# Optimization experiments

Hardware: AMD Instinct MI355X
Metric: run time of the kernel (lower is better)

The kernel has to match this reference:

```python
import jax, jax.numpy as jnp
import numpy as np

IN_DIM, R = 80, 5
MEL = IN_DIM * R          # 400
H = 256                   # hidden size used everywhere
PRE2 = 128                # prenet second layer
B, T_ENC, T_DEC = 16, 384, 200


def _gru(x, h, wih, whh, bih, bhh):
    """torch.nn.GRUCell math."""
    gi = x @ wih.T + bih
    gh = h @ whh.T + bhh
    ir, iz, inn = jnp.split(gi, 3, axis=-1)
    hr, hz, hn = jnp.split(gh, 3, axis=-1)
    r = jax.nn.sigmoid(ir + hr)
    z = jax.nn.sigmoid(iz + hz)
    n = jnp.tanh(inn + r * hn)
    return (1.0 - z) * n + z * h


def setup_inputs() -> dict:
    key = jax.random.key(0)
    ks = jax.random.split(key, 32)
    p = lambda k, shape: jax.random.normal(k, shape, dtype=jnp.float32) * 0.05
    inp = {
        "encoder_outputs": jax.random.normal(ks[0], (B, T_ENC, H), dtype=jnp.float32),
        "inputs": jax.random.normal(ks[1], (B, T_DEC, MEL), dtype=jnp.float32),
        "memory_lengths": jax.random.randint(ks[2], (B,), T_ENC // 2, T_ENC + 1, dtype=jnp.int32),
        # prenet: Linear(400,256) -> relu -> Linear(256,128) -> relu (dropout omitted = eval mode)
        "prenet_w1": p(ks[3], (H, MEL)), "prenet_b1": p(ks[4], (H,)),
        "prenet_w2": p(ks[5], (PRE2, H)), "prenet_b2": p(ks[6], (PRE2,)),
        # memory_layer: Linear(256,256,bias=False)
        "mem_w": p(ks[7], (H, H)),
        # attention GRUCell(256+128 -> 256)
        "attn_gru_wih": p(ks[8], (3 * H, H + PRE2)), "attn_gru_whh": p(ks[9], (3 * H, H)),
        "attn_gru_bih": p(ks[10], (3 * H,)), "attn_gru_bhh": p(ks[11], (3 * H,)),
        # BahdanauAttention: query_layer Linear(256,256,bias=False), v Linear(256,1,bias=False)
        "attn_q_w": p(ks[12], (H, H)), "attn_v": p(ks[13], (H,)),
        # project_to_decoder_in: Linear(512,256)
        "proj_in_w": p(ks[14], (H, 2 * H)), "proj_in_b": p(ks[15], (H,)),
        # two decoder GRUCells(256,256), stacked on leading axis
        "dec_wih": p(ks[16], (2, 3 * H, H)), "dec_whh": p(ks[17], (2, 3 * H, H)),
        "dec_bih": p(ks[18], (2, 3 * H)), "dec_bhh": p(ks[19], (2, 3 * H)),
        # proj_to_mel: Linear(256,400)
        "mel_w": p(ks[20], (MEL, H)), "mel_b": p(ks[21], (MEL,)),
    }
    return inp


def reference(encoder_outputs, inputs, memory_lengths,
              prenet_w1, prenet_b1, prenet_w2, prenet_b2, mem_w,
              attn_gru_wih, attn_gru_whh, attn_gru_bih, attn_gru_bhh,
              attn_q_w, attn_v, proj_in_w, proj_in_b,
              dec_wih, dec_whh, dec_bih, dec_bhh, mel_w, mel_b):
    b, t_enc, d = encoder_outputs.shape
    processed_memory = encoder_outputs @ mem_w.T                # (B,T_enc,256)
    pad_mask = jnp.arange(t_enc)[None, :] >= memory_lengths[:, None]  # True = padded

    # teacher forcing: step t consumes inputs[t-1], step 0 consumes zeros
    shifted = jnp.concatenate([jnp.zeros_like(inputs[:, :1]), inputs[:, :-1]], axis=1)
    xs = jnp.swapaxes(shifted, 0, 1)                            # (T_dec,B,400)

    def step(carry, x):
        attn_h, attention, d1, d2 = carry
        # prenet (eval mode: dropout disabled)
        pn = jax.nn.relu(x @ prenet_w1.T + prenet_b1)
        pn = jax.nn.relu(pn @ prenet_w2.T + prenet_b2)           # (B,128)
        # attention GRU cell on [prenet_out, prev_attention]
        cell_in = jnp.concatenate([pn, attention], axis=-1)      # (B,384)
        attn_h = _gru(cell_in, attn_h, attn_gru_wih, attn_gru_whh,
                      attn_gru_bih, attn_gru_bhh)                # (B,256)
        # Bahdanau additive attention
        pq = attn_h @ attn_q_w.T                                 # (B,256)
        e = jnp.tanh(pq[:, None, :] + processed_memory) @ attn_v  # (B,T_enc)
        e = jnp.where(pad_mask, -jnp.inf, e)
        align = jax.nn.softmax(e, axis=-1)
        attention = jnp.einsum('bt,btd->bd', align, encoder_outputs)  # (B,256)
        # decoder input projection + 2 residual GRU cells
        dec_in = jnp.concatenate([attn_h, attention], axis=-1) @ proj_in_w.T + proj_in_b
        hs = [d1, d2]
        for i in range(2):
            hs[i] = _gru(dec_in, hs[i], dec_wih[i], dec_whh[i], dec_bih[i], dec_bhh[i])
            dec_in = hs[i] + dec_in
        out = dec_in @ mel_w.T + mel_b                           # (B,400)
        return (attn_h, attention, hs[0], hs[1]), (out, align)

    z = jnp.zeros((b, d), dtype=encoder_outputs.dtype)
    init = (z, z, z, z)
    _, (outs, aligns) = jax.lax.scan(step, init, xs)
    outputs = jnp.swapaxes(outs, 0, 1)                           # (B,T_dec,400)
    alignments = jnp.swapaxes(aligns, 0, 1)                      # (B,T_dec,T_enc)
    return outputs, alignments
```

## Files before the change

kernel.cpp:

```cpp
#include <hip/hip_runtime.h>
#include <math.h>

#define TID ((int)threadIdx.x)
#define BID ((int)blockIdx.x)

typedef float4 f4;

constexpr int NB   = 16;
constexpr int TENC = 384;
constexpr int TDEC = 200;
constexpr int HD   = 256;
constexpr int MELD = 400;
constexpr int P2   = 128;
constexpr int G3   = 768;

constexpr int OFF_PM     = 0;
constexpr int OFF_GIPN   = OFF_PM     + NB*TENC*HD;
constexpr int OFF_PN1    = OFF_GIPN   + TDEC*G3*NB;
constexpr int OFF_PN2    = OFF_PN1    + TDEC*HD*NB;
constexpr int OFF_D2O    = OFF_PN2    + TDEC*P2*NB;
constexpr int OFF_ATTNH  = OFF_D2O    + TDEC*HD*NB;
constexpr int OFF_CTX    = OFF_ATTNH  + 2*4096;
constexpr int OFF_D1     = OFF_CTX    + 3*4096;
constexpr int OFF_D2     = OFF_D1     + 2*4096;
constexpr int OFF_DECIN  = OFF_D2     + 4096;
constexpr int OFF_DECIN1 = OFF_DECIN  + 4096;
constexpr int OFF_GI     = OFF_DECIN1 + 4096;
constexpr int OFF_GH     = OFF_GI     + 12288;
constexpr int OFF_GI1    = OFF_GH     + 12288;
constexpr int OFF_GH1    = OFF_GI1    + 12288;
constexpr int OFF_GI2    = OFF_GH1    + 12288;
constexpr int OFF_GH2    = OFF_GI2    + 12288;
constexpr int OFF_PQ     = OFF_GH2    + 12288;
constexpr int OFF_E      = OFF_PQ     + 4096;
constexpr int OFF_W1T    = OFF_E      + 6144;
constexpr int OFF_W2T    = OFF_W1T    + 102400;
constexpr int OFF_WMEMT  = OFF_W2T    + 32768;
constexpr int OFF_WPNT   = OFF_WMEMT  + 65536;
constexpr int OFF_WATTT  = OFF_WPNT   + 98304;
constexpr int OFF_WHHT   = OFF_WATTT  + 196608;
constexpr int OFF_WQT    = OFF_WHHT   + 196608;
constexpr int OFF_WPROJT = OFF_WQT    + 65536;
constexpr int OFF_WIH1T  = OFF_WPROJT + 131072;
constexpr int OFF_WHH1T  = OFF_WIH1T  + 196608;
constexpr int OFF_WIH2T  = OFF_WHH1T  + 196608;
constexpr int OFF_WHH2T  = OFF_WIH2T  + 196608;
constexpr int OFF_WMELT  = OFF_WHH2T  + 196608;

__device__ __forceinline__ float sigf(float x){ return 1.f/(1.f+__expf(-x)); }
__device__ __forceinline__ float tanhf_(float x){
  x = fminf(15.f, fmaxf(-15.f, x));
  float e = __expf(2.f*x);
  return (e-1.f)/(e+1.f);
}

__global__ void k_init(float* ws){
  int g = BID*256 + TID;
  for (int idx = g; idx < 32768; idx += 32*256) ws[OFF_ATTNH + idx] = 0.f;
}

__global__ void k_tr(const float* pw1, const float* pw2, const float* wmem,
                     const float* gwih, const float* gwhh, const float* qw,
                     const float* pjw, const float* dwih, const float* dwhh,
                     const float* mw, float* ws){
  int g = BID*256 + TID;
  if (g < 102400){ int j=g%256,k=g/256; ws[OFF_W1T+g]=pw1[j*400+k]; return;} g-=102400;
  if (g < 32768){ int j=g%128,k=g/128; ws[OFF_W2T+g]=pw2[j*256+k]; return;} g-=32768;
  if (g < 65536){ int j=g%256,k=g/256; ws[OFF_WMEMT+g]=wmem[j*256+k]; return;} g-=65536;
  if (g < 98304){ int j=g%768,k=g/768; ws[OFF_WPNT+g]=gwih[j*384+k]; return;} g-=98304;
  if (g < 196608){ int j=g%768,k=g/768; ws[OFF_WATTT+g]=gwih[j*384+128+k]; return;} g-=196608;
  if (g < 196608){ int j=g%768,k=g/768; ws[OFF_WHHT+g]=gwhh[j*256+k]; return;} g-=196608;
  if (g < 65536){ int j=g%256,k=g/256; ws[OFF_WQT+g]=qw[j*256+k]; return;} g-=65536;
  if (g < 131072){ int j=g%256,k=g/256; ws[OFF_WPROJT+g]=pjw[j*512+k]; return;} g-=131072;
  if (g < 196608){ int j=g%768,k=g/768; ws[OFF_WIH1T+g]=dwih[j*256+k]; return;} g-=196608;
  if (g < 196608){ int j=g%768,k=g/768; ws[OFF_WHH1T+g]=dwhh[j*256+k]; return;} g-=196608;
  if (g < 196608){ int j=g%768,k=g/768; ws[OFF_WIH2T+g]=dwih[196608+j*256+k]; return;} g-=196608;
  if (g < 196608){ int j=g%768,k=g/768; ws[OFF_WHH2T+g]=dwhh[196608+j*256+k]; return;} g-=196608;
  if (g < 102400){ int j=g%400,k=g/400; ws[OFF_WMELT+g]=mw[j*256+k]; return;}
}

__global__ void k_pm(const float* __restrict__ enc, float* __restrict__ ws){
  int b = BID / 24, t0 = (BID % 24) * 16;
  int d = TID;
  const float* W = ws + OFF_WMEMT + d;
  const float* A = enc + (size_t)(b*TENC + t0)*HD;
  float acc[16];
  #pragma unroll
  for (int tt=0; tt<16; ++tt) acc[tt]=0.f;
  for (int k=0; k<HD; k+=4){
    float w0=W[(k+0)*256], w1=W[(k+1)*256], w2=W[(k+2)*256], w3=W[(k+3)*256];
    #pragma unroll
    for (int tt=0; tt<16; ++tt){
      f4 a = *(const f4*)(A + tt*HD + k);
      acc[tt] += w0*a.x + w1*a.y + w2*a.z + w3*a.w;
    }
  }
  float* P = ws + OFF_PM + (size_t)(b*TENC + t0)*HD + d;
  #pragma unroll
  for (int tt=0; tt<16; ++tt) P[tt*HD] = acc[tt];
}

__global__ void k_pre1(const float* __restrict__ inp, const float* __restrict__ pb1, float* __restrict__ ws){
  int t = BID >> 2;
  int j = ((BID & 3) * 64) + (TID & 63);
  int bq = TID >> 6;
  float b = pb1[j];
  float a0=b,a1=b,a2=b,a3=b;
  if (t > 0){
    const float* W = ws + OFF_W1T + j;
    const float* x0 = inp + (size_t)((bq*4+0)*TDEC + (t-1))*MELD;
    const float* x1 = inp + (size_t)((bq*4+1)*TDEC + (t-1))*MELD;
    const float* x2 = inp + (size_t)((bq*4+2)*TDEC + (t-1))*MELD;
    const float* x3 = inp + (size_t)((bq*4+3)*TDEC + (t-1))*MELD;
    for (int k=0;k<MELD;k+=4){
      float w0=W[(k+0)*256],w1=W[(k+1)*256],w2=W[(k+2)*256],w3=W[(k+3)*256];
      f4 v0=*(const f4*)(x0+k), v1=*(const f4*)(x1+k), v2=*(const f4*)(x2+k), v3=*(const f4*)(x3+k);
      a0 += w0*v0.x+w1*v0.y+w2*v0.z+w3*v0.w;
      a1 += w0*v1.x+w1*v1.y+w2*v1.z+w3*v1.w;
      a2 += w0*v2.x+w1*v2.y+w2*v2.z+w3*v2.w;
      a3 += w0*v3.x+w1*v3.y+w2*v3.z+w3*v3.w;
    }
  }
  f4 r; r.x=fmaxf(a0,0.f); r.y=fmaxf(a1,0.f); r.z=fmaxf(a2,0.f); r.w=fmaxf(a3,0.f);
  *(f4*)(ws + OFF_PN1 + (size_t)(t*HD + j)*NB + bq*4) = r;
}

__global__ void k_pre2(const float* __restrict__ pb2, float* __restrict__ ws){
  int t = BID >> 1;
  int j = ((BID & 1) * 64) + (TID & 63);
  int bq = TID >> 6;
  float b = pb2[j];
  f4 acc = {b,b,b,b};
  const float* W = ws + OFF_W2T + j;
  const float* A = ws + OFF_PN1 + (size_t)t*HD*NB + bq*4;
  #pragma unroll 4
  for (int k=0;k<HD;++k){
    float w = W[k*P2];
    f4 a = *(const f4*)(A + k*NB);
    acc.x += w*a.x; acc.y += w*a.y; acc.z += w*a.z; acc.w += w*a.w;
  }
  f4 r; r.x=fmaxf(acc.x,0.f); r.y=fmaxf(acc.y,0.f); r.z=fmaxf(acc.z,0.f); r.w=fmaxf(acc.w,0.f);
  *(f4*)(ws + OFF_PN2 + (size_t)(t*P2 + j)*NB + bq*4) = r;
}

__global__ void k_gipn(const float* __restrict__ gbih, float* __restrict__ ws){
  int t = BID / 12;
  int j = (BID % 12)*64 + (TID & 63);
  int bq = TID >> 6;
  float b = gbih[j];
  f4 acc = {b,b,b,b};
  const float* W = ws + OFF_WPNT + j;
  const float* A = ws + OFF_PN2 + (size_t)t*P2*NB + bq*4;
  #pragma unroll 4
  for (int k=0;k<P2;++k){
    float w = W[k*G3];
    f4 a = *(const f4*)(A + k*NB);
    acc.x += w*a.x; acc.y += w*a.y; acc.z += w*a.z; acc.w += w*a.w;
  }
  *(f4*)(ws + OFF_GIPN + (size_t)(t*G3 + j)*NB + bq*4) = acc;
}

__global__ void k1(float* __restrict__ ws, const float* __restrict__ gbhh,
                   const float* __restrict__ pjb, const float* __restrict__ dbhh, int i){
  __shared__ float as[4096];
  int lane = TID & 63, bq = TID >> 6;
  if (BID < 12){
    if (i >= TDEC) return;
    const float* cp = ws + OFF_CTX;
    #pragma unroll
    for (int e=0;e<16;++e){ int id = TID + e*256; as[id] = cp[id] + cp[id+4096] + cp[id+8192]; }
    __syncthreads();
    int j = BID*64 + lane;
    f4 acc = *(const f4*)(ws + OFF_GIPN + ((size_t)i*G3 + j)*NB + bq*4);
    const float* W = ws + OFF_WATTT + j;
    #pragma unroll 4
    for (int k=0;k<HD;++k){
      float w = W[k*G3];
      f4 a = *(const f4*)&as[k*NB + bq*4];
      acc.x += w*a.x; acc.y += w*a.y; acc.z += w*a.z; acc.w += w*a.w;
    }
    *(f4*)(ws + OFF_GI + j*NB + bq*4) = acc;
  } else if (BID < 24){
    if (i >= TDEC) return;
    int j = (BID-12)*64 + lane;
    float bb = gbhh[j];
    f4 acc = {bb,bb,bb,bb};
    const float* W = ws + OFF_WHHT + j;
    const float* A = ws + OFF_ATTNH + ((i+1)&1)*4096 + bq*4;
    #pragma unroll 4
    for (int k=0;k<HD;++k){
      float w = W[k*G3];
      f4 a = *(const f4*)(A + k*NB);
      acc.x += w*a.x; acc.y += w*a.y; acc.z += w*a.z; acc.w += w*a.w;
    }
    *(f4*)(ws + OFF_GH + j*NB + bq*4) = acc;
  } else if (BID < 28){
    if (i == 0) return;
    const float* cp = ws + OFF_CTX;
    #pragma unroll
    for (int e=0;e<16;++e){ int id = TID + e*256; as[id] = cp[id] + cp[id+4096] + cp[id+8192]; }
    __syncthreads();
    int row = (BID-24)*64 + lane;
    float bb = pjb[row];
    f4 acc = {bb,bb,bb,bb};
    const float* W = ws + OFF_WPROJT + row;
    const float* Ah = ws + OFF_ATTNH + ((i+1)&1)*4096 + bq*4;
    #pragma unroll 4
    for (int k=0;k<HD;++k){
      float w = W[k*HD];
      f4 a = *(const f4*)(Ah + k*NB);
      acc.x += w*a.x; acc.y += w*a.y; acc.z += w*a.z; acc.w += w*a.w;
    }
    #pragma unroll 4
    for (int k=0;k<HD;++k){
      float w = W[(k+HD)*HD];
      f4 a = *(const f4*)&as[k*NB + bq*4];
      acc.x += w*a.x; acc.y += w*a.y; acc.z += w*a.z; acc.w += w*a.w;
    }
    *(f4*)(ws + OFF_DECIN + row*NB + bq*4) = acc;
  } else if (BID < 40){
    if (i == 0) return;
    int j = (BID-28)*64 + lane;
    float bb = dbhh[G3 + j];
    f4 acc = {bb,bb,bb,bb};
    const float* W = ws + OFF_WHH2T + j;
    const float* A = ws + OFF_D2 + bq*4;
    #pragma unroll 4
    for (int k=0;k<HD;++k){
      float w = W[k*G3];
      f4 a = *(const f4*)(A + k*NB);
      acc.x += w*a.x; acc.y += w*a.y; acc.z += w*a.z; acc.w += w*a.w;
    }
    *(f4*)(ws + OFF_GH2 + j*NB + bq*4) = acc;
  }
}

__global__ void k2(float* __restrict__ ws, const float* __restrict__ dbih, int i){
  __shared__ float attns[4096];
  int lane = TID & 63, bq = TID >> 6;
  if (BID < 4){
    if (i >= TDEC) return;
    const float* gi = ws + OFF_GI; const float* gh = ws + OFF_GH;
    const float* hp = ws + OFF_ATTNH + ((i+1)&1)*4096;
    float* hn = ws + OFF_ATTNH + (i&1)*4096;
    #pragma unroll
    for (int e=0;e<16;++e){
      int id = TID + e*256;
      float ir=gi[id], iz=gi[id+4096], in_=gi[id+8192];
      float hr=gh[id], hz=gh[id+4096], hnn=gh[id+8192];
      float h = hp[id];
      float rr = sigf(ir+hr), zz = sigf(iz+hz);
      float nn = tanhf_(in_ + rr*hnn);
      float v = (1.f-zz)*nn + zz*h;
      attns[id] = v;
      if (BID==0) hn[id] = v;
    }
    __syncthreads();
    int row = BID*64 + lane;
    const float* W = ws + OFF_WQT + row;
    float a0=0.f,a1=0.f,a2=0.f,a3=0.f;
    #pragma unroll 4
    for (int k=0;k<HD;++k){
      float w = W[k*HD];
      f4 a = *(const f4*)&attns[k*NB + bq*4];
      a0 += w*a.x; a1 += w*a.y; a2 += w*a.z; a3 += w*a.w;
    }
    float* pq = ws + OFF_PQ;
    pq[(bq*4+0)*HD+row]=a0; pq[(bq*4+1)*HD+row]=a1;
    pq[(bq*4+2)*HD+row]=a2; pq[(bq*4+3)*HD+row]=a3;
  } else {
    if (i == 0) return;
    int j = (BID-4)*64 + lane;
    float bb = dbih[j];
    f4 acc = {bb,bb,bb,bb};
    const float* W = ws + OFF_WIH1T + j;
    const float* A = ws + OFF_DECIN + bq*4;
    #pragma unroll 4
    for (int k=0;k<HD;++k){
      float w = W[k*G3];
      f4 a = *(const f4*)(A + k*NB);
      acc.x += w*a.x; acc.y += w*a.y; acc.z += w*a.z; acc.w += w*a.w;
    }
    *(f4*)(ws + OFF_GI1 + j*NB + bq*4) = acc;
  }
}

__global__ void k4(float* __restrict__ ws, const float* __restrict__ av,
                   const int* __restrict__ mlen, const float* __restrict__ dbih, int i){
  __shared__ float sh[4096];
  if (BID < 48){
    if (i >= TDEC) return;
    int b = BID/3, ts = BID%3;
    int ks = TID >> 7, tt = TID & 127;
    int t = ts*128 + tt;
    const float* pmr = ws + OFF_PM + (size_t)(b*TENC + t)*HD + ks*128;
    const float* pqb = ws + OFF_PQ + b*HD + ks*128;
    const float* vv = av + ks*128;
    float s = 0.f;
    #pragma unroll 4
    for (int d=0; d<128; d+=4){
      f4 p = *(const f4*)(pmr+d);
      f4 q = *(const f4*)(pqb+d);
      f4 w = *(const f4*)(vv+d);
      s += w.x*tanhf_(p.x+q.x) + w.y*tanhf_(p.y+q.y)
         + w.z*tanhf_(p.z+q.z) + w.w*tanhf_(p.w+q.w);
    }
    sh[TID] = s; __syncthreads();
    if (TID < 128){
      float e = sh[TID] + sh[TID+128];
      int len = mlen[b];
      int tw = ts*128 + TID;
      ws[OFF_E + b*TENC + tw] = (tw < len) ? e : -1e30f;
    }
  } else {
    if (i == 0) return;
    int lane = TID & 63, bq = TID >> 6;
    const float* gi1 = ws + OFF_GI1; const float* gh1 = ws + OFF_GH1;
    const float* d1p = ws + OFF_D1 + (i&1)*4096;
    float* d1n = ws + OFF_D1 + ((i+1)&1)*4096;
    const float* din = ws + OFF_DECIN;
    float* din1 = ws + OFF_DECIN1;
    #pragma unroll
    for (int e=0;e<16;++e){
      int id = TID + e*256;
      float ir=gi1[id], iz=gi1[id+4096], in_=gi1[id+8192];
      float hr=gh1[id], hz=gh1[id+4096], hnn=gh1[id+8192];
      float h = d1p[id];
      float rr=sigf(ir+hr), zz=sigf(iz+hz);
      float nn=tanhf_(in_+rr*hnn);
      float dn = (1.f-zz)*nn + zz*h;
      float v = dn + din[id];
      sh[id] = v;
      if (BID==48){ d1n[id]=dn; din1[id]=v; }
    }
    __syncthreads();
    int j = (BID-48)*64 + lane;
    float bb = dbih[G3 + j];
    f4 acc = {bb,bb,bb,bb};
    const float* W = ws + OFF_WIH2T + j;
    #pragma unroll 4
    for (int k=0;k<HD;++k){
      float w = W[k*G3];
      f4 a = *(const f4*)&sh[k*NB + bq*4];
      acc.x += w*a.x; acc.y += w*a.y; acc.z += w*a.z; acc.w += w*a.w;
    }
    *(f4*)(ws + OFF_GI2 + j*NB + bq*4) = acc;
  }
}

__global__ void k5(float* __restrict__ ws, const float* __restrict__ enc,
                   const float* __restrict__ dbhh, float* __restrict__ out, int i){
  __shared__ float red[256];
  __shared__ float ps[128];
  if (BID < 48){
    if (i >= TDEC) return;
    int b = BID/3, ts = BID%3;
    const float* eb = ws + OFF_E + b*TENC;
    float m = -1e30f;
    for (int idx=TID; idx<TENC; idx+=256) m = fmaxf(m, eb[idx]);
    red[TID]=m; __syncthreads();
    for (int s=128; s>0; s>>=1){ if (TID<s) red[TID]=fmaxf(red[TID],red[TID+s]); __syncthreads(); }
    float M = red[0]; __syncthreads();
    float sl = 0.f;
    for (int idx=TID; idx<TENC; idx+=256) sl += __expf(eb[idx]-M);
    red[TID]=sl; __syncthreads();
    for (int s=128; s>0; s>>=1){ if (TID<s) red[TID]+=red[TID+s]; __syncthreads(); }
    float inv = 1.f/red[0];
    __syncthreads();
    if (TID < 128){
      int t = ts*128 + TID;
      float p = __expf(eb[t]-M)*inv;
      ps[TID] = p;
      out[1280000 + (size_t)(b*TDEC + i)*TENC + t] = p;
    }
    __syncthreads();
    const float* encb = enc + (size_t)(b*TENC + ts*128)*HD + TID;
    float ctx = 0.f;
    #pragma unroll 8
    for (int tt=0;tt<128;++tt) ctx += ps[tt]*encb[(size_t)tt*HD];
    ws[OFF_CTX + ts*4096 + TID*NB + b] = ctx;
  } else if (BID < 52){
    if (i == 0) return;
    const float* gi2 = ws+OFF_GI2; const float* gh2 = ws+OFF_GH2;
    float* d2 = ws+OFF_D2; const float* din1 = ws+OFF_DECIN1;
    float* d2o = ws + OFF_D2O + (size_t)(i-1)*4096;
    #pragma unroll
    for (int e=0;e<4;++e){
      int id = (BID-48)*1024 + e*256 + TID;
      float ir=gi2[id], iz=gi2[id+4096], in_=gi2[id+8192];
      float hr=gh2[id], hz=gh2[id+4096], hnn=gh2[id+8192];
      float h = d2[id];
      float rr=sigf(ir+hr), zz=sigf(iz+hz);
      float nn=tanhf_(in_+rr*hnn);
      float dn=(1.f-zz)*nn+zz*h;
      d2[id]=dn;
      d2o[id]=dn+din1[id];
    }
  } else {
    if (i >= TDEC) return;
    int lane=TID&63, bq=TID>>6;
    int j = (BID-52)*64 + lane;
    float bb = dbhh[j];
    f4 acc = {bb,bb,bb,bb};
    const float* W = ws+OFF_WHH1T+j;
    const float* A = ws+OFF_D1+((i+1)&1)*4096+bq*4;
    #pragma unroll 4
    for (int k=0;k<HD;++k){
      float w = W[k*G3];
      f4 a = *(const f4*)(A + k*NB);
      acc.x += w*a.x; acc.y += w*a.y; acc.z += w*a.z; acc.w += w*a.w;
    }
    *(f4*)(ws + OFF_GH1 + j*NB + bq*4) = acc;
  }
}

__global__ void k_mel(const float* __restrict__ ws, const float* __restrict__ mb, float* __restrict__ out){
  int t = BID/7, rb = (BID%7)*64;
  int j = rb + (TID&63), bq = TID>>6;
  if (j >= MELD) return;
  float bb = mb[j];
  f4 acc = {bb,bb,bb,bb};
  const float* W = ws + OFF_WMELT + j;
  const float* A = ws + OFF_D2O + (size_t)t*4096 + bq*4;
  #pragma unroll 4
  for (int k=0;k<HD;++k){
    float w = W[k*MELD];
    f4 a = *(const f4*)(A + k*NB);
    acc.x += w*a.x; acc.y += w*a.y; acc.z += w*a.z; acc.w += w*a.w;
  }
  out[(size_t)(bq*4+0)*80000 + t*MELD + j] = acc.x;
  out[(size_t)(bq*4+1)*80000 + t*MELD + j] = acc.y;
  out[(size_t)(bq*4+2)*80000 + t*MELD + j] = acc.z;
  out[(size_t)(bq*4+3)*80000 + t*MELD + j] = acc.w;
}

extern "C" void kernel_launch(void* const* d_in, const int* in_sizes, int n_in,
                              void* d_out, int out_size, void* d_ws, size_t ws_size,
                              hipStream_t stream) {
  const float* enc  = (const float*)d_in[0];
  const float* inp  = (const float*)d_in[1];
  const int*   mlen = (const int*)  d_in[2];
  const float* pw1  = (const float*)d_in[3];
  const float* pb1  = (const float*)d_in[4];
  const float* pw2  = (const float*)d_in[5];
  const float* pb2  = (const float*)d_in[6];
  const float* wmem = (const float*)d_in[7];
  const float* gwih = (const float*)d_in[8];
  const float* gwhh = (const float*)d_in[9];
  const float* gbih = (const float*)d_in[10];
  const float* gbhh = (const float*)d_in[11];
  const float* qw   = (const float*)d_in[12];
  const float* av   = (const float*)d_in[13];
  const float* pjw  = (const float*)d_in[14];
  const float* pjb  = (const float*)d_in[15];
  const float* dwih = (const float*)d_in[16];
  const float* dwhh = (const float*)d_in[17];
  const float* dbih = (const float*)d_in[18];
  const float* dbhh = (const float*)d_in[19];
  const float* mw   = (const float*)d_in[20];
  const float* mb   = (const float*)d_in[21];
  float* ws  = (float*)d_ws;
  float* out = (float*)d_out;

  k_init<<<32,256,0,stream>>>(ws);
  k_tr  <<<6944,256,0,stream>>>(pw1,pw2,wmem,gwih,gwhh,qw,pjw,dwih,dwhh,mw,ws);
  k_pm  <<<384,256,0,stream>>>(enc, ws);
  k_pre1<<<800,256,0,stream>>>(inp, pb1, ws);
  k_pre2<<<400,256,0,stream>>>(pb2, ws);
  k_gipn<<<2400,256,0,stream>>>(gbih, ws);
  for (int i = 0; i <= TDEC; ++i){
    k1<<<40,256,0,stream>>>(ws, gbhh, pjb, dbhh, i);
    k2<<<16,256,0,stream>>>(ws, dbih, i);
    k4<<<60,256,0,stream>>>(ws, av, mlen, dbih, i);
    k5<<<64,256,0,stream>>>(ws, enc, dbhh, out, i);
  }
  k_mel<<<1400,256,0,stream>>>(ws, mb, out);
}
```

Baseline: 18.96 ms.

## Replace per-step kernel launches with one persistent kernel using grid barriers

The 804 small per-timestep launches are replaced by a single persistent kernel of 72 blocks that loops over all decoder steps. Phases are separated by an atomic-counter grid barrier, and the decoder GRU stages are software-pipelined across iterations with double-buffered state. The query projection is also fused into the attention-energy blocks, and sigmoid/tanh now use hardware exp2/rcp intrinsics. This removes launch overhead and inter-kernel gaps, but it relies on all 72 blocks being co-resident and adds spin-wait barrier latency.

```diff
diff --git a/kernel.cpp b/kernel.cpp
--- a/kernel.cpp
+++ b/kernel.cpp
@@ -13,6 +13,7 @@
 constexpr int MELD = 400;
 constexpr int P2   = 128;
 constexpr int G3   = 768;
+constexpr int NBLK = 72;
 
 constexpr int OFF_PM     = 0;
 constexpr int OFF_GIPN   = OFF_PM     + NB*TENC*HD;
@@ -23,17 +24,17 @@
 constexpr int OFF_CTX    = OFF_ATTNH  + 2*4096;
 constexpr int OFF_D1     = OFF_CTX    + 3*4096;
 constexpr int OFF_D2     = OFF_D1     + 2*4096;
-constexpr int OFF_DECIN  = OFF_D2     + 4096;
-constexpr int OFF_DECIN1 = OFF_DECIN  + 4096;
-constexpr int OFF_GI     = OFF_DECIN1 + 4096;
+constexpr int OFF_BAR    = OFF_D2     + 4096;
+constexpr int OFF_DECIN  = OFF_BAR    + 256;
+constexpr int OFF_DECIN1 = OFF_DECIN  + 2*4096;
+constexpr int OFF_GI     = OFF_DECIN1 + 2*4096;
 constexpr int OFF_GH     = OFF_GI     + 12288;
 constexpr int OFF_GI1    = OFF_GH     + 12288;
 constexpr int OFF_GH1    = OFF_GI1    + 12288;
 constexpr int OFF_GI2    = OFF_GH1    + 12288;
 constexpr int OFF_GH2    = OFF_GI2    + 12288;
-constexpr int OFF_PQ     = OFF_GH2    + 12288;
-constexpr int OFF_E      = OFF_PQ     + 4096;
-constexpr int OFF_W1T    = OFF_E      + 6144;
+constexpr int OFF_E      = OFF_GH2    + 12288;
+constexpr int OFF_W1T    = OFF_E      + NB*TENC;
 constexpr int OFF_W2T    = OFF_W1T    + 102400;
 constexpr int OFF_WMEMT  = OFF_W2T    + 32768;
 constexpr int OFF_WPNT   = OFF_WMEMT  + 65536;
@@ -47,16 +48,29 @@
 constexpr int OFF_WHH2T  = OFF_WIH2T  + 196608;
 constexpr int OFF_WMELT  = OFF_WHH2T  + 196608;
 
-__device__ __forceinline__ float sigf(float x){ return 1.f/(1.f+__expf(-x)); }
-__device__ __forceinline__ float tanhf_(float x){
-  x = fminf(15.f, fmaxf(-15.f, x));
-  float e = __expf(2.f*x);
-  return (e-1.f)/(e+1.f);
+__device__ __forceinline__ float fexp2(float x){ return __builtin_amdgcn_exp2f(x); }
+__device__ __forceinline__ float frcp(float x){ return __builtin_amdgcn_rcpf(x); }
+__device__ __forceinline__ float sigf(float x){ return frcp(1.f + fexp2(-1.44269504f*x)); }
+__device__ __forceinline__ float tanhf_(float x){ return 1.f - 2.f*frcp(1.f + fexp2(2.88539008f*x)); }
+
+__device__ __forceinline__ void gridbar(float* ws, unsigned target_iters){
+  unsigned* cnt = (unsigned*)(ws + OFF_BAR);
+  __syncthreads();
+  if (TID == 0){
+    __threadfence();
+    __hip_atomic_fetch_add(cnt, 1u, __ATOMIC_RELEASE, __HIP_MEMORY_SCOPE_AGENT);
+    unsigned target = target_iters * NBLK;
+    while (__hip_atomic_load(cnt, __ATOMIC_ACQUIRE, __HIP_MEMORY_SCOPE_AGENT) < target){
+      __builtin_amdgcn_s_sleep(1);
+    }
+    __threadfence();
+  }
+  __syncthreads();
 }
 
 __global__ void k_init(float* ws){
   int g = BID*256 + TID;
-  for (int idx = g; idx < 32768; idx += 32*256) ws[OFF_ATTNH + idx] = 0.f;
+  for (int idx = g; idx < 33024; idx += 32*256) ws[OFF_ATTNH + idx] = 0.f;
 }
 
 __global__ void k_tr(const float* pw1, const float* pw2, const float* wmem,
@@ -160,257 +174,259 @@
   *(f4*)(ws + OFF_GIPN + (size_t)(t*G3 + j)*NB + bq*4) = acc;
 }
 
-__global__ void k1(float* __restrict__ ws, const float* __restrict__ gbhh,
-                   const float* __restrict__ pjb, const float* __restrict__ dbhh, int i){
-  __shared__ float as[4096];
-  int lane = TID & 63, bq = TID >> 6;
-  if (BID < 12){
-    if (i >= TDEC) return;
-    const float* cp = ws + OFF_CTX;
-    #pragma unroll
-    for (int e=0;e<16;++e){ int id = TID + e*256; as[id] = cp[id] + cp[id+4096] + cp[id+8192]; }
-    __syncthreads();
-    int j = BID*64 + lane;
-    f4 acc = *(const f4*)(ws + OFF_GIPN + ((size_t)i*G3 + j)*NB + bq*4);
-    const float* W = ws + OFF_WATTT + j;
-    #pragma unroll 4
-    for (int k=0;k<HD;++k){
-      float w = W[k*G3];
-      f4 a = *(const f4*)&as[k*NB + bq*4];
-      acc.x += w*a.x; acc.y += w*a.y; acc.z += w*a.z; acc.w += w*a.w;
-    }
-    *(f4*)(ws + OFF_GI + j*NB + bq*4) = acc;
-  } else if (BID < 24){
-    if (i >= TDEC) return;
-    int j = (BID-12)*64 + lane;
-    float bb = gbhh[j];
-    f4 acc = {bb,bb,bb,bb};
-    const float* W = ws + OFF_WHHT + j;
-    const float* A = ws + OFF_ATTNH + ((i+1)&1)*4096 + bq*4;
-    #pragma unroll 4
-    for (int k=0;k<HD;++k){
-      float w = W[k*G3];
-      f4 a = *(const f4*)(A + k*NB);
-      acc.x += w*a.x; acc.y += w*a.y; acc.z += w*a.z; acc.w += w*a.w;
-    }
-    *(f4*)(ws + OFF_GH + j*NB + bq*4) = acc;
-  } else if (BID < 28){
-    if (i == 0) return;
-    const float* cp = ws + OFF_CTX;
-    #pragma unroll
-    for (int e=0;e<16;++e){ int id = TID + e*256; as[id] = cp[id] + cp[id+4096] + cp[id+8192]; }
-    __syncthreads();
-    int row = (BID-24)*64 + lane;
-    float bb = pjb[row];
-    f4 acc = {bb,bb,bb,bb};
-    const float* W = ws + OFF_WPROJT + row;
-    const float* Ah = ws + OFF_ATTNH + ((i+1)&1)*4096 + bq*4;
-    #pragma unroll 4
-    for (int k=0;k<HD;++k){
-      float w = W[k*HD];
-      f4 a = *(const f4*)(Ah + k*NB);
-      acc.x += w*a.x; acc.y += w*a.y; acc.z += w*a.z; acc.w += w*a.w;
-    }
-    #pragma unroll 4
-    for (int k=0;k<HD;++k){
-      float w = W[(k+HD)*HD];
-      f4 a = *(const f4*)&as[k*NB + bq*4];
-      acc.x += w*a.x; acc.y += w*a.y; acc.z += w*a.z; acc.w += w*a.w;
-    }
-    *(f4*)(ws + OFF_DECIN + row*NB + bq*4) = acc;
-  } else if (BID < 40){
-    if (i == 0) return;
-    int j = (BID-28)*64 + lane;
-    float bb = dbhh[G3 + j];
-    f4 acc = {bb,bb,bb,bb};
-    const float* W = ws + OFF_WHH2T + j;
-    const float* A = ws + OFF_D2 + bq*4;
-    #pragma unroll 4
-    for (int k=0;k<HD;++k){
-      float w = W[k*G3];
-      f4 a = *(const f4*)(A + k*NB);
-      acc.x += w*a.x; acc.y += w*a.y; acc.z += w*a.z; acc.w += w*a.w;
-    }
-    *(f4*)(ws + OFF_GH2 + j*NB + bq*4) = acc;
-  }
-}
-
-__global__ void k2(float* __restrict__ ws, const float* __restrict__ dbih, int i){
-  __shared__ float attns[4096];
-  int lane = TID & 63, bq = TID >> 6;
-  if (BID < 4){
-    if (i >= TDEC) return;
-    const float* gi = ws + OFF_GI; const float* gh = ws + OFF_GH;
-    const float* hp = ws + OFF_ATTNH + ((i+1)&1)*4096;
-    float* hn = ws + OFF_ATTNH + (i&1)*4096;
-    #pragma unroll
-    for (int e=0;e<16;++e){
-      int id = TID + e*256;
-      float ir=gi[id], iz=gi[id+4096], in_=gi[id+8192];
-      float hr=gh[id], hz=gh[id+4096], hnn=gh[id+8192];
-      float h = hp[id];
-      float rr = sigf(ir+hr), zz = sigf(iz+hz);
-      float nn = tanhf_(in_ + rr*hnn);
-      float v = (1.f-zz)*nn + zz*h;
-      attns[id] = v;
-      if (BID==0) hn[id] = v;
-    }
-    __syncthreads();
-    int row = BID*64 + lane;
-    const float* W = ws + OFF_WQT + row;
-    float a0=0.f,a1=0.f,a2=0.f,a3=0.f;
-    #pragma unroll 4
-    for (int k=0;k<HD;++k){
-      float w = W[k*HD];
-      f4 a = *(const f4*)&attns[k*NB + bq*4];
-      a0 += w*a.x; a1 += w*a.y; a2 += w*a.z; a3 += w*a.w;
-    }
-    float* pq = ws + OFF_PQ;
-    pq[(bq*4+0)*HD+row]=a0; pq[(bq*4+1)*HD+row]=a1;
-    pq[(bq*4+2)*HD+row]=a2; pq[(bq*4+3)*HD+row]=a3;
-  } else {
-    if (i == 0) return;
-    int j = (BID-4)*64 + lane;
-    float bb = dbih[j];
-    f4 acc = {bb,bb,bb,bb};
-    const float* W = ws + OFF_WIH1T + j;
-    const float* A = ws + OFF_DECIN + bq*4;
-    #pragma unroll 4
-    for (int k=0;k<HD;++k){
-      float w = W[k*G3];
-      f4 a = *(const f4*)(A + k*NB);
-      acc.x += w*a.x; acc.y += w*a.y; acc.z += w*a.z; acc.w += w*a.w;
-    }
-    *(f4*)(ws + OFF_GI1 + j*NB + bq*4) = acc;
-  }
-}
-
-__global__ void k4(float* __restrict__ ws, const float* __restrict__ av,
-                   const int* __restrict__ mlen, const float* __restrict__ dbih, int i){
+__global__ void __launch_bounds__(256, 1)
+k_loop(float* __restrict__ ws, const float* __restrict__ enc,
+       const float* __restrict__ av, const int* __restrict__ mlen,
+       const float* __restrict__ gbhh, const float* __restrict__ pjb,
+       const float* __restrict__ dbih, const float* __restrict__ dbhh,
+       float* __restrict__ out){
   __shared__ float sh[4096];
-  if (BID < 48){
-    if (i >= TDEC) return;
-    int b = BID/3, ts = BID%3;
-    int ks = TID >> 7, tt = TID & 127;
-    int t = ts*128 + tt;
-    const float* pmr = ws + OFF_PM + (size_t)(b*TENC + t)*HD + ks*128;
-    const float* pqb = ws + OFF_PQ + b*HD + ks*128;
-    const float* vv = av + ks*128;
-    float s = 0.f;
-    #pragma unroll 4
-    for (int d=0; d<128; d+=4){
-      f4 p = *(const f4*)(pmr+d);
-      f4 q = *(const f4*)(pqb+d);
-      f4 w = *(const f4*)(vv+d);
-      s += w.x*tanhf_(p.x+q.x) + w.y*tanhf_(p.y+q.y)
-         + w.z*tanhf_(p.z+q.z) + w.w*tanhf_(p.w+q.w);
-    }
-    sh[TID] = s; __syncthreads();
-    if (TID < 128){
-      float e = sh[TID] + sh[TID+128];
-      int len = mlen[b];
-      int tw = ts*128 + TID;
-      ws[OFF_E + b*TENC + tw] = (tw < len) ? e : -1e30f;
-    }
-  } else {
-    if (i == 0) return;
-    int lane = TID & 63, bq = TID >> 6;
-    const float* gi1 = ws + OFF_GI1; const float* gh1 = ws + OFF_GH1;
-    const float* d1p = ws + OFF_D1 + (i&1)*4096;
-    float* d1n = ws + OFF_D1 + ((i+1)&1)*4096;
-    const float* din = ws + OFF_DECIN;
-    float* din1 = ws + OFF_DECIN1;
-    #pragma unroll
-    for (int e=0;e<16;++e){
-      int id = TID + e*256;
-      float ir=gi1[id], iz=gi1[id+4096], in_=gi1[id+8192];
-      float hr=gh1[id], hz=gh1[id+4096], hnn=gh1[id+8192];
-      float h = d1p[id];
-      float rr=sigf(ir+hr), zz=sigf(iz+hz);
-      float nn=tanhf_(in_+rr*hnn);
-      float dn = (1.f-zz)*nn + zz*h;
-      float v = dn + din[id];
-      sh[id] = v;
-      if (BID==48){ d1n[id]=dn; din1[id]=v; }
-    }
-    __syncthreads();
-    int j = (BID-48)*64 + lane;
-    float bb = dbih[G3 + j];
-    f4 acc = {bb,bb,bb,bb};
-    const float* W = ws + OFF_WIH2T + j;
-    #pragma unroll 4
-    for (int k=0;k<HD;++k){
-      float w = W[k*G3];
-      f4 a = *(const f4*)&sh[k*NB + bq*4];
-      acc.x += w*a.x; acc.y += w*a.y; acc.z += w*a.z; acc.w += w*a.w;
-    }
-    *(f4*)(ws + OFF_GI2 + j*NB + bq*4) = acc;
-  }
-}
-
-__global__ void k5(float* __restrict__ ws, const float* __restrict__ enc,
-                   const float* __restrict__ dbhh, float* __restrict__ out, int i){
-  __shared__ float red[256];
-  __shared__ float ps[128];
-  if (BID < 48){
-    if (i >= TDEC) return;
-    int b = BID/3, ts = BID%3;
-    const float* eb = ws + OFF_E + b*TENC;
-    float m = -1e30f;
-    for (int idx=TID; idx<TENC; idx+=256) m = fmaxf(m, eb[idx]);
-    red[TID]=m; __syncthreads();
-    for (int s=128; s>0; s>>=1){ if (TID<s) red[TID]=fmaxf(red[TID],red[TID+s]); __syncthreads(); }
-    float M = red[0]; __syncthreads();
-    float sl = 0.f;
-    for (int idx=TID; idx<TENC; idx+=256) sl += __expf(eb[idx]-M);
-    red[TID]=sl; __syncthreads();
-    for (int s=128; s>0; s>>=1){ if (TID<s) red[TID]+=red[TID+s]; __syncthreads(); }
-    float inv = 1.f/red[0];
-    __syncthreads();
-    if (TID < 128){
-      int t = ts*128 + TID;
-      float p = __expf(eb[t]-M)*inv;
-      ps[TID] = p;
-      out[1280000 + (size_t)(b*TDEC + i)*TENC + t] = p;
-    }
-    __syncthreads();
-    const float* encb = enc + (size_t)(b*TENC + ts*128)*HD + TID;
-    float ctx = 0.f;
-    #pragma unroll 8
-    for (int tt=0;tt<128;++tt) ctx += ps[tt]*encb[(size_t)tt*HD];
-    ws[OFF_CTX + ts*4096 + TID*NB + b] = ctx;
-  } else if (BID < 52){
-    if (i == 0) return;
-    const float* gi2 = ws+OFF_GI2; const float* gh2 = ws+OFF_GH2;
-    float* d2 = ws+OFF_D2; const float* din1 = ws+OFF_DECIN1;
-    float* d2o = ws + OFF_D2O + (size_t)(i-1)*4096;
-    #pragma unroll
-    for (int e=0;e<4;++e){
-      int id = (BID-48)*1024 + e*256 + TID;
-      float ir=gi2[id], iz=gi2[id+4096], in_=gi2[id+8192];
-      float hr=gh2[id], hz=gh2[id+4096], hnn=gh2[id+8192];
-      float h = d2[id];
-      float rr=sigf(ir+hr), zz=sigf(iz+hz);
-      float nn=tanhf_(in_+rr*hnn);
-      float dn=(1.f-zz)*nn+zz*h;
-      d2[id]=dn;
-      d2o[id]=dn+din1[id];
-    }
-  } else {
-    if (i >= TDEC) return;
-    int lane=TID&63, bq=TID>>6;
-    int j = (BID-52)*64 + lane;
-    float bb = dbhh[j];
-    f4 acc = {bb,bb,bb,bb};
-    const float* W = ws+OFF_WHH1T+j;
-    const float* A = ws+OFF_D1+((i+1)&1)*4096+bq*4;
-    #pragma unroll 4
-    for (int k=0;k<HD;++k){
-      float w = W[k*G3];
-      f4 a = *(const f4*)(A + k*NB);
-      acc.x += w*a.x; acc.y += w*a.y; acc.z += w*a.z; acc.w += w*a.w;
-    }
-    *(f4*)(ws + OFF_GH1 + j*NB + bq*4) = acc;
+  const int bid = BID;
+  const int lane = TID & 63, bq = TID >> 6;
+  unsigned nbar = 0;
+
+  for (int i = 0; i <= TDEC + 2; ++i){
+    if (bid < 12){
+      const float* cp = ws + OFF_CTX;
+      #pragma unroll
+      for (int e=0;e<16;++e){ int id=TID+e*256; sh[id]=cp[id]+cp[id+4096]+cp[id+8192]; }
+      __syncthreads();
+      if (i < TDEC){
+        int j = bid*64 + lane;
+        f4 acc = *(const f4*)(ws + OFF_GIPN + ((size_t)i*G3 + j)*NB + bq*4);
+        const float* W = ws + OFF_WATTT + j;
+        #pragma unroll 4
+        for (int k=0;k<HD;++k){
+          float w = W[k*G3];
+          f4 a = *(const f4*)&sh[k*NB + bq*4];
+          acc.x += w*a.x; acc.y += w*a.y; acc.z += w*a.z; acc.w += w*a.w;
+        }
+        *(f4*)(ws + OFF_GI + j*NB + bq*4) = acc;
+      }
+    } else if (bid < 24){
+      if (i < TDEC){
+        int j = (bid-12)*64 + lane;
+        float bb = gbhh[j];
+        f4 acc = {bb,bb,bb,bb};
+        const float* W = ws + OFF_WHHT + j;
+        const float* A = ws + OFF_ATTNH + ((i+1)&1)*4096 + bq*4;
+        #pragma unroll 4
+        for (int k=0;k<HD;++k){
+          float w = W[k*G3];
+          f4 a = *(const f4*)(A + k*NB);
+          acc.x += w*a.x; acc.y += w*a.y; acc.z += w*a.z; acc.w += w*a.w;
+        }
+        *(f4*)(ws + OFF_GH + j*NB + bq*4) = acc;
+      }
+    } else if (bid < 28){
+      const float* cp = ws + OFF_CTX;
+      #pragma unroll
+      for (int e=0;e<16;++e){ int id=TID+e*256; sh[id]=cp[id]+cp[id+4096]+cp[id+8192]; }
+      __syncthreads();
+      if (i >= 1 && i <= TDEC){
+        int row = (bid-24)*64 + lane;
+        float bb = pjb[row];
+        f4 acc = {bb,bb,bb,bb};
+        const float* W = ws + OFF_WPROJT + row;
+        const float* Ah = ws + OFF_ATTNH + ((i+1)&1)*4096 + bq*4;
+        #pragma unroll 4
+        for (int k=0;k<HD;++k){
+          float w = W[k*HD];
+          f4 a = *(const f4*)(Ah + k*NB);
+          acc.x += w*a.x; acc.y += w*a.y; acc.z += w*a.z; acc.w += w*a.w;
+        }
+        #pragma unroll 4
+        for (int k=0;k<HD;++k){
+          float w = W[(k+HD)*HD];
+          f4 a = *(const f4*)&sh[k*NB + bq*4];
+          acc.x += w*a.x; acc.y += w*a.y; acc.z += w*a.z; acc.w += w*a.w;
+        }
+        *(f4*)(ws + OFF_DECIN + ((i-1)&1)*4096 + row*NB + bq*4) = acc;
+      }
+    } else if (bid == 28){
+      if (i >= 2 && i <= TDEC+1){
+        const float* gi1 = ws + OFF_GI1;
+        const float* gh1 = ws + OFF_GH1;
+        const float* hp  = ws + OFF_D1 + ((i+1)&1)*4096;
+        float*       d1n = ws + OFF_D1 + (i&1)*4096;
+        const float* din = ws + OFF_DECIN  + (i&1)*4096;
+        float*       dn1 = ws + OFF_DECIN1 + (i&1)*4096;
+        #pragma unroll
+        for (int e=0;e<16;++e){
+          int id = TID + e*256;
+          float ir=gi1[id], iz=gi1[id+4096], in_=gi1[id+8192];
+          float hr=gh1[id], hz=gh1[id+4096], hnn=gh1[id+8192];
+          float h = hp[id];
+          float rr=sigf(ir+hr), zz=sigf(iz+hz);
+          float nn=tanhf_(in_+rr*hnn);
+          float dn=(1.f-zz)*nn+zz*h;
+          d1n[id]=dn;
+          dn1[id]=dn+din[id];
+        }
+      }
+    } else if (bid == 29){
+      if (i >= 3){
+        const float* gi2 = ws + OFF_GI2;
+        const float* gh2 = ws + OFF_GH2;
+        float*       d2  = ws + OFF_D2;
+        const float* dn1 = ws + OFF_DECIN1 + ((i+1)&1)*4096;
+        float*       d2o = ws + OFF_D2O + (size_t)(i-3)*4096;
+        #pragma unroll
+        for (int e=0;e<16;++e){
+          int id = TID + e*256;
+          float ir=gi2[id], iz=gi2[id+4096], in_=gi2[id+8192];
+          float hr=gh2[id], hz=gh2[id+4096], hnn=gh2[id+8192];
+          float h = d2[id];
+          float rr=sigf(ir+hr), zz=sigf(iz+hz);
+          float nn=tanhf_(in_+rr*hnn);
+          float dn=(1.f-zz)*nn+zz*h;
+          d2[id]=dn;
+          d2o[id]=dn+dn1[id];
+        }
+      }
+    }
+    gridbar(ws, ++nbar);
+
+    if (bid < 48){
+      if (i < TDEC){
+        int b = bid/3, ts = bid%3;
+        {
+          int d = TID, id = d*NB + b;
+          const float* gi = ws + OFF_GI; const float* gh = ws + OFF_GH;
+          float h = ws[OFF_ATTNH + ((i+1)&1)*4096 + id];
+          float ir=gi[id], iz=gi[id+4096], in_=gi[id+8192];
+          float hr=gh[id], hz=gh[id+4096], hnn=gh[id+8192];
+          float rr=sigf(ir+hr), zz=sigf(iz+hz);
+          float nn=tanhf_(in_+rr*hnn);
+          float v=(1.f-zz)*nn+zz*h;
+          sh[d]=v;
+          if (ts==0) ws[OFF_ATTNH + (i&1)*4096 + id]=v;
+        }
+        __syncthreads();
+        {
+          int d = TID;
+          const float* W = ws + OFF_WQT + d;
+          float p = 0.f;
+          #pragma unroll 4
+          for (int k=0;k<HD;++k) p += W[k*HD]*sh[k];
+          sh[256+d]=p;
+        }
+        __syncthreads();
+        {
+          int ks = TID>>7, tt = TID&127, t = ts*128+tt;
+          const float* pmr = ws + OFF_PM + ((size_t)(b*TENC + t))*HD + ks*128;
+          const float* q  = &sh[256 + ks*128];
+          const float* vv = av + ks*128;
+          float s = 0.f;
+          #pragma unroll 4
+          for (int d0=0; d0<128; d0+=4){
+            f4 p = *(const f4*)(pmr+d0);
+            f4 w = *(const f4*)(vv+d0);
+            s += w.x*tanhf_(p.x+q[d0+0]) + w.y*tanhf_(p.y+q[d0+1])
+               + w.z*tanhf_(p.z+q[d0+2]) + w.w*tanhf_(p.w+q[d0+3]);
+          }
+          sh[512+TID]=s;
+        }
+        __syncthreads();
+        if (TID < 128){
+          float e = sh[512+TID] + sh[512+TID+128];
+          int len = mlen[bid/3];
+          int tw = (bid%3)*128 + TID;
+          ws[OFF_E + (bid/3)*TENC + tw] = (tw < len) ? e : -1e30f;
+        }
+      }
+    } else if (bid < 60){
+      if (i >= 1 && i <= TDEC){
+        int j = (bid-48)*64 + lane;
+        float bb = dbih[j];
+        f4 acc = {bb,bb,bb,bb};
+        const float* W = ws + OFF_WIH1T + j;
+        const float* A = ws + OFF_DECIN + ((i-1)&1)*4096 + bq*4;
+        #pragma unroll 4
+        for (int k=0;k<HD;++k){
+          float w = W[k*G3];
+          f4 a = *(const f4*)(A + k*NB);
+          acc.x += w*a.x; acc.y += w*a.y; acc.z += w*a.z; acc.w += w*a.w;
+        }
+        *(f4*)(ws + OFF_GI1 + j*NB + bq*4) = acc;
+      }
+    } else {
+      if (i >= 1 && i <= TDEC+1){
+        int j = (bid-60)*64 + lane;
+        float bb = dbhh[j];
+        f4 acc = {bb,bb,bb,bb};
+        const float* W = ws + OFF_WHH1T + j;
+        const float* A = ws + OFF_D1 + (i&1)*4096 + bq*4;
+        #pragma unroll 4
+        for (int k=0;k<HD;++k){
+          float w = W[k*G3];
+          f4 a = *(const f4*)(A + k*NB);
+          acc.x += w*a.x; acc.y += w*a.y; acc.z += w*a.z; acc.w += w*a.w;
+        }
+        *(f4*)(ws + OFF_GH1 + j*NB + bq*4) = acc;
+      }
+    }
+    gridbar(ws, ++nbar);
+
+    if (bid < 48){
+      if (i < TDEC){
+        int b = bid/3, ts = bid%3;
+        const float* eb = ws + OFF_E + b*TENC;
+        float m = -1e30f;
+        for (int idx=TID; idx<TENC; idx+=256) m = fmaxf(m, eb[idx]);
+        sh[TID]=m; __syncthreads();
+        for (int s=128; s>0; s>>=1){ if (TID<s) sh[TID]=fmaxf(sh[TID],sh[TID+s]); __syncthreads(); }
+        float M = sh[0]; __syncthreads();
+        float sl = 0.f;
+        for (int idx=TID; idx<TENC; idx+=256) sl += fexp2(1.44269504f*(eb[idx]-M));
+        sh[TID]=sl; __syncthreads();
+        for (int s=128; s>0; s>>=1){ if (TID<s) sh[TID]+=sh[TID+s]; __syncthreads(); }
+        float inv = frcp(sh[0]); __syncthreads();
+        if (TID < 128){
+          int t = ts*128 + TID;
+          float p = fexp2(1.44269504f*(eb[t]-M))*inv;
+          sh[256+TID] = p;
+          out[1280000 + (size_t)(b*TDEC + i)*TENC + t] = p;
+        }
+        __syncthreads();
+        const float* encb = enc + ((size_t)(b*TENC + ts*128))*HD + TID;
+        float ctx = 0.f;
+        #pragma unroll 8
+        for (int tt=0;tt<128;++tt) ctx += sh[256+tt]*encb[(size_t)tt*HD];
+        ws[OFF_CTX + ts*4096 + TID*NB + b] = ctx;
+      }
+    } else if (bid < 60){
+      if (i >= 2 && i <= TDEC+1){
+        int j = (bid-48)*64 + lane;
+        float bb = dbih[G3 + j];
+        f4 acc = {bb,bb,bb,bb};
+        const float* W = ws + OFF_WIH2T + j;
+        const float* A = ws + OFF_DECIN1 + (i&1)*4096 + bq*4;
+        #pragma unroll 4
+        for (int k=0;k<HD;++k){
+          float w = W[k*G3];
+          f4 a = *(const f4*)(A + k*NB);
+          acc.x += w*a.x; acc.y += w*a.y; acc.z += w*a.z; acc.w += w*a.w;
+        }
+        *(f4*)(ws + OFF_GI2 + j*NB + bq*4) = acc;
+      }
+    } else {
+      if (i >= 2 && i <= TDEC+1){
+        int j = (bid-60)*64 + lane;
+        float bb = dbhh[G3 + j];
+        f4 acc = {bb,bb,bb,bb};
+        const float* W = ws + OFF_WHH2T + j;
+        const float* A = ws + OFF_D2 + bq*4;
+        #pragma unroll 4
+        for (int k=0;k<HD;++k){
+          float w = W[k*G3];
+          f4 a = *(const f4*)(A + k*NB);
+          acc.x += w*a.x; acc.y += w*a.y; acc.z += w*a.z; acc.w += w*a.w;
+        }
+        *(f4*)(ws + OFF_GH2 + j*NB + bq*4) = acc;
+      }
+    }
+    gridbar(ws, ++nbar);
   }
 }
 
@@ -468,11 +484,8 @@
   k_pre1<<<800,256,0,stream>>>(inp, pb1, ws);
   k_pre2<<<400,256,0,stream>>>(pb2, ws);
   k_gipn<<<2400,256,0,stream>>>(gbih, ws);
-  for (int i = 0; i <= TDEC; ++i){
-    k1<<<40,256,0,stream>>>(ws, gbhh, pjb, dbhh, i);
-    k2<<<16,256,0,stream>>>(ws, dbih, i);
-    k4<<<60,256,0,stream>>>(ws, av, mlen, dbih, i);
-    k5<<<64,256,0,stream>>>(ws, enc, dbhh, out, i);
-  }
+
+  k_loop<<<NBLK,256,0,stream>>>(ws, enc, av, mlen, gbhh, pjb, dbih, dbhh, out);
+
   k_mel<<<1400,256,0,stream>>>(ws, mb, out);
 }
```

New measurement: 72.26 ms. 281% more time.
